# Kernel tuning notes

Measured on AMD Instinct MI355X. Metric: run time of the kernel, lower is better.

## Reference

```python
import jax, jax.numpy as jnp
import numpy as np

# dims (match init_kwargs / input_specs)
IN = 128      # input_size / num_features
GH = 512      # global_hidden_size
GL = 3        # global_nlayers
NH = 128      # effective noise hidden (DFRNN kwarg noise_nlayers, due to arg swap)
NL = 2        # effective noise layers (DFRNN kwarg noise_hidden_size, due to arg swap)
NF = 10       # n_global_factors
NT = 1024     # num_ts
T = 192       # num_periods


def _cell(x, W, bi, bh):
    # single LSTM step from zero state: c0=h0=0 => f-gate and W_hh drop out
    g = x @ W.T + bi + bh                      # [n, 4H]
    i, f, c, o = jnp.split(g, 4, axis=-1)      # torch gate order i,f,g,o
    cc = jax.nn.sigmoid(i) * jnp.tanh(c)
    return jax.nn.sigmoid(o) * jnp.tanh(cc)


def _stack(x, Wih0, bih0, bhh0, Wih, bih, bhh):
    h = _cell(x, Wih0, bih0, bhh0)
    for l in range(Wih.shape[0]):              # small fixed layer count
        h = _cell(h, Wih[l], bih[l], bhh[l])
    return h


def setup_inputs() -> dict:
    key = jax.random.key(0)
    ks = jax.random.split(key, 16)
    s = 0.05
    return {
        "X": jax.random.normal(ks[0], (NT, T, IN), jnp.float32),
        # global-factor LSTM params
        "g_Wih0": s * jax.random.normal(ks[1], (4 * GH, IN), jnp.float32),
        "g_bih0": s * jax.random.normal(ks[2], (4 * GH,), jnp.float32),
        "g_bhh0": s * jax.random.normal(ks[3], (4 * GH,), jnp.float32),
        "g_Wih": s * jax.random.normal(ks[4], (GL - 1, 4 * GH, GH), jnp.float32),
        "g_bih": s * jax.random.normal(ks[5], (GL - 1, 4 * GH), jnp.float32),
        "g_bhh": s * jax.random.normal(ks[6], (GL - 1, 4 * GH), jnp.float32),
        # embed linear (global_hidden_size -> n_global_factors)
        "e_W": s * jax.random.normal(ks[7], (NF, GH), jnp.float32),
        "e_b": s * jax.random.normal(ks[8], (NF,), jnp.float32),
        # noise LSTM params
        "n_Wih0": s * jax.random.normal(ks[9], (4 * NH, IN), jnp.float32),
        "n_bih0": s * jax.random.normal(ks[10], (4 * NH,), jnp.float32),
        "n_bhh0": s * jax.random.normal(ks[11], (4 * NH,), jnp.float32),
        "n_Wih": s * jax.random.normal(ks[12], (NL - 1, 4 * NH, NH), jnp.float32),
        "n_bih": s * jax.random.normal(ks[13], (NL - 1, 4 * NH), jnp.float32),
        "n_bhh": s * jax.random.normal(ks[14], (NL - 1, 4 * NH), jnp.float32),
        # noise affine head (NH -> 1)
        "a_W": s * jax.random.normal(ks[15], (1, NH), jnp.float32),
        "a_b": jnp.zeros((1,), jnp.float32),
    }


def reference(X, g_Wih0, g_bih0, g_bhh0, g_Wih, g_bih, g_bhh, e_W, e_b,
              n_Wih0, n_bih0, n_bhh0, n_Wih, n_bih, n_bhh, a_W, a_b):
    nt, t, f = X.shape
    Z = X.reshape(nt * t, f)                                   # all (ts, period) tokens, loop vectorized
    # DeepFactor branch: gt = relu(last-layer h), factor linear is dead code
    gt = jax.nn.relu(_stack(Z, g_Wih0, g_bih0, g_bhh0, g_Wih, g_bih, g_bhh))
    mu = (gt @ e_W.T + e_b).sum(axis=-1).reshape(nt, t)        # embed then sum over factors
    # Noise branch
    hn = jax.nn.relu(_stack(Z, n_Wih0, n_bih0, n_bhh0, n_Wih, n_bih, n_bhh))
    st = hn @ a_W.T + a_b                                      # [nt*t, 1]
    sigma = jnp.log1p(jnp.exp(st)).reshape(nt, t) + 1e-6       # log(1+exp) + eps
    return mu, sigma
```

## Files before the change

kernel.cpp:

```cpp
#include <hip/hip_runtime.h>

#define IN_F  128
#define GHID  512
#define NHID  128
#define NTOK  196608L
#define LDSP  520

#define L2E 1.4426950408889634f

typedef __attribute__((ext_vector_type(8))) short short8;
typedef __attribute__((ext_vector_type(4))) float floatx4;
typedef __attribute__((ext_vector_type(4))) float f4;

#define O_GW0 0L
#define O_GW1 196608L
#define O_GW2 983040L
#define O_NW0 1769472L
#define O_NW1 1818624L
#define NWS   1867776L
#define F_GB0 0
#define F_GB1 1536
#define F_GB2 3072
#define F_NB0 4608
#define F_NB1 4992
#define F_WE  5376
#define F_AW  5888
#define F_BE  6016
#define F_AB  6017

__device__ __forceinline__ unsigned short f2bf(float f) {
  unsigned int u = __float_as_uint(f);
  u += 0x7fffu + ((u >> 16) & 1u);
  return (unsigned short)(u >> 16);
}

__device__ __forceinline__ long srcoff(long pp, int H, int K) {
  long f = pp >> 9;
  int r = (int)(pp & 511);
  int ln = r >> 3, j = r & 7;
  int nKT = K >> 5, nCT = H >> 4;
  int tk = (int)(f % nKT);
  long t2 = f / nKT;
  int tn = (int)(t2 % nCT);
  int gate = (int)(t2 / nCT);
  int n = tn * 16 + (ln & 15);
  int k = tk * 32 + ((ln >> 4) << 3) + j;
  int go = (gate == 0) ? 0 : ((gate == 1) ? 2 * H : 3 * H);
  return (long)(go + n) * K + k;
}

__global__ void prep_kernel(
    const float* __restrict__ gW0, const float* __restrict__ gbi0, const float* __restrict__ gbh0,
    const float* __restrict__ gW,  const float* __restrict__ gbi,  const float* __restrict__ gbh,
    const float* __restrict__ eW,  const float* __restrict__ eb,
    const float* __restrict__ nW0, const float* __restrict__ nbi0, const float* __restrict__ nbh0,
    const float* __restrict__ nW,  const float* __restrict__ nbi,  const float* __restrict__ nbh,
    const float* __restrict__ aW,  const float* __restrict__ ab,
    unsigned short* __restrict__ wpk, float* __restrict__ fpk)
{
  long idx = (long)blockIdx.x * blockDim.x + threadIdx.x;
  if (idx < NWS) {
    const float* src;
    long off;
    if (idx < O_GW1)      { off = srcoff(idx - O_GW0, 512, 128); src = gW0; }
    else if (idx < O_GW2) { off = srcoff(idx - O_GW1, 512, 512); src = gW; }
    else if (idx < O_NW0) { off = srcoff(idx - O_GW2, 512, 512); src = gW + 1048576; }
    else if (idx < O_NW1) { off = srcoff(idx - O_NW0, 128, 128); src = nW0; }
    else                  { off = srcoff(idx - O_NW1, 128, 128); src = nW; }
    wpk[idx] = f2bf(src[off]);
    return;
  }
  long p = idx - NWS;
  if (p < 1536) { int g = (int)(p >> 9), n = (int)(p & 511);
    int o = (g == 0 ? 0 : (g == 1 ? 1024 : 1536)) + n;
    fpk[F_GB0 + p] = gbi0[o] + gbh0[o]; return; }
  p -= 1536;
  if (p < 1536) { int g = (int)(p >> 9), n = (int)(p & 511);
    int o = (g == 0 ? 0 : (g == 1 ? 1024 : 1536)) + n;
    fpk[F_GB1 + p] = gbi[o] + gbh[o]; return; }
  p -= 1536;
  if (p < 1536) { int g = (int)(p >> 9), n = (int)(p & 511);
    int o = (g == 0 ? 0 : (g == 1 ? 1024 : 1536)) + n;
    fpk[F_GB2 + p] = gbi[2048 + o] + gbh[2048 + o]; return; }
  p -= 1536;
  if (p < 384) { int g = (int)(p / 128), n = (int)(p % 128);
    int o = (g == 0 ? 0 : (g == 1 ? 256 : 384)) + n;
    fpk[F_NB0 + p] = nbi0[o] + nbh0[o]; return; }
  p -= 384;
  if (p < 384) { int g = (int)(p / 128), n = (int)(p % 128);
    int o = (g == 0 ? 0 : (g == 1 ? 256 : 384)) + n;
    fpk[F_NB1 + p] = nbi[o] + nbh[o]; return; }
  p -= 384;
  if (p < 512) { float s = 0.f;
    for (int f = 0; f < 10; ++f) s += eW[f * 512 + p];
    fpk[F_WE + p] = s; return; }
  p -= 512;
  if (p < 128) { fpk[F_AW + p] = aW[p]; return; }
  p -= 128;
  if (p == 0) { float s = 0.f; for (int f = 0; f < 10; ++f) s += eb[f]; fpk[F_BE] = s; return; }
  if (p == 1) { fpk[F_AB] = ab[0]; return; }
}

__device__ __forceinline__ float cell_h(float gi, float gc, float go) {
  float ei = __builtin_amdgcn_exp2f(gi * -L2E);
  float u  = __builtin_amdgcn_exp2f(gc * (2.0f * L2E));
  float eo = __builtin_amdgcn_exp2f(go * -L2E);
  float r1 = __builtin_amdgcn_rcpf((u + 1.f) * (1.f + ei));
  float cc = (u - 1.f) * r1;
  float s  = cc * cc;
  float num = cc * fmaf(10.f, s, 105.f);
  float den = fmaf(s, s + 45.f, 105.f);
  return num * __builtin_amdgcn_rcpf(den * (1.f + eo));
}

template <int K, int H, int TT, int CPW, int NW, int MODE>
__device__ __forceinline__ void layer_run(
    const unsigned short* __restrict__ sIn,
    unsigned short* __restrict__ sOut,
    const unsigned short* __restrict__ wp,
    const float* __restrict__ bias,
    const float* __restrict__ dotw,
    float* accVec,
    int colTile0, int tokBase, int lane)
{
  constexpr int nKT = K / 32;
  constexpr int nCT = H / 16;
#pragma unroll
  for (int cp = 0; cp < CPW; ++cp) {
    int tn = colTile0 + cp * NW;
    int colBase = tn * 16 + ((lane >> 4) << 2);
    const unsigned short* p0 = wp + (size_t)tn * nKT * 512 + lane * 8;
    const unsigned short* p1 = p0 + (size_t)nCT * nKT * 512;
    const unsigned short* p2 = p1 + (size_t)nCT * nKT * 512;
    short8 b0 = *(const short8*)(p0);
    short8 b1 = *(const short8*)(p1);
    short8 b2 = *(const short8*)(p2);
    f4 bi4 = *(const f4*)(bias + colBase);
    f4 bc4 = *(const f4*)(bias + H + colBase);
    f4 bo4 = *(const f4*)(bias + 2 * H + colBase);
    floatx4 acc[3][TT];
#pragma unroll
    for (int tt = 0; tt < TT; ++tt) {
      acc[0][tt] = (floatx4){bi4.x, bi4.y, bi4.z, bi4.w};
      acc[1][tt] = (floatx4){bc4.x, bc4.y, bc4.z, bc4.w};
      acc[2][tt] = (floatx4){bo4.x, bo4.y, bo4.z, bo4.w};
    }
    const unsigned short* aRow = sIn + (size_t)(tokBase + (lane & 15)) * LDSP + ((lane >> 4) << 3);
#pragma unroll 1
    for (int ks = 0; ks < nKT; ++ks) {
      int nks = (ks + 1 < nKT) ? (ks + 1) : ks;
      short8 nb0 = *(const short8*)(p0 + (size_t)nks * 512);
      short8 nb1 = *(const short8*)(p1 + (size_t)nks * 512);
      short8 nb2 = *(const short8*)(p2 + (size_t)nks * 512);
      short8 a[TT];
#pragma unroll
      for (int tt = 0; tt < TT; ++tt)
        a[tt] = *(const short8*)(aRow + (size_t)tt * 16 * LDSP + ks * 32);
#pragma unroll
      for (int tt = 0; tt < TT; ++tt) {
        acc[0][tt] = __builtin_amdgcn_mfma_f32_16x16x32_bf16(b0, a[tt], acc[0][tt], 0, 0, 0);
        acc[1][tt] = __builtin_amdgcn_mfma_f32_16x16x32_bf16(b1, a[tt], acc[1][tt], 0, 0, 0);
        acc[2][tt] = __builtin_amdgcn_mfma_f32_16x16x32_bf16(b2, a[tt], acc[2][tt], 0, 0, 0);
      }
      b0 = nb0; b1 = nb1; b2 = nb2;
    }
    f4 dw4;
    if constexpr (MODE == 1) dw4 = *(const f4*)(dotw + colBase);
#pragma unroll
    for (int tt = 0; tt < TT; ++tt) {
      int token = tokBase + tt * 16 + (lane & 15);
      if constexpr (MODE == 0) {
        ushort4 hw;
        hw.x = f2bf(cell_h(acc[0][tt][0], acc[1][tt][0], acc[2][tt][0]));
        hw.y = f2bf(cell_h(acc[0][tt][1], acc[1][tt][1], acc[2][tt][1]));
        hw.z = f2bf(cell_h(acc[0][tt][2], acc[1][tt][2], acc[2][tt][2]));
        hw.w = f2bf(cell_h(acc[0][tt][3], acc[1][tt][3], acc[2][tt][3]));
        *(ushort4*)&sOut[(size_t)token * LDSP + colBase] = hw;
      } else {
        float v = 0.f;
#pragma unroll
        for (int r = 0; r < 4; ++r) {
          float h = cell_h(acc[0][tt][r], acc[1][tt][r], acc[2][tt][r]);
          v = fmaf(fmaxf(h, 0.f), dw4[r], v);
        }
        v += __shfl_xor(v, 16);
        v += __shfl_xor(v, 32);
        if (lane < 16) atomicAdd(&accVec[token], v);
      }
    }
  }
}

__attribute__((amdgpu_waves_per_eu(4, 4)))
__global__ __launch_bounds__(1024) void dfrnn_main(
    const float* __restrict__ X,
    const unsigned short* __restrict__ wpk,
    const float* __restrict__ fpk,
    float* __restrict__ out)
{
  __shared__ __align__(16) unsigned short bufA[64 * LDSP];
  __shared__ __align__(16) unsigned short bufB[64 * LDSP];
  __shared__ float accMu[64];
  __shared__ float accSt[64];
  int tid = threadIdx.x;
  int wave = tid >> 6, lane = tid & 63;
  size_t blkTok = (size_t)blockIdx.x * 64;

  if (tid < 64) { accMu[tid] = 0.f; accSt[tid] = 0.f; }
  for (int i = tid; i < 64 * 32; i += 1024) {
    int row = i >> 5, c4 = i & 31;
    f4 v = __builtin_nontemporal_load((const f4*)(X + (blkTok + row) * 128 + c4 * 4));
    ushort4 b;
    b.x = f2bf(v.x); b.y = f2bf(v.y); b.z = f2bf(v.z); b.w = f2bf(v.w);
    *(ushort4*)&bufA[(size_t)row * LDSP + c4 * 4] = b;
  }
  __syncthreads();

  layer_run<128, 128, 2, 1, 8, 0>(bufA, bufA + 128, wpk + O_NW0, fpk + F_NB0,
                                  nullptr, nullptr, wave & 7, (wave >> 3) * 32, lane);
  __syncthreads();

  layer_run<128, 128, 2, 1, 8, 1>(bufA + 128, nullptr, wpk + O_NW1, fpk + F_NB1,
                                  fpk + F_AW, accSt, wave & 7, (wave >> 3) * 32, lane);
  layer_run<128, 512, 4, 2, 16, 0>(bufA, bufB, wpk + O_GW0, fpk + F_GB0,
                                   nullptr, nullptr, wave, 0, lane);
  __syncthreads();

  layer_run<512, 512, 4, 2, 16, 0>(bufB, bufA, wpk + O_GW1, fpk + F_GB1,
                                   nullptr, nullptr, wave, 0, lane);
  __syncthreads();

  layer_run<512, 512, 4, 2, 16, 1>(bufA, nullptr, wpk + O_GW2, fpk + F_GB2,
                                   fpk + F_WE, accMu, wave, 0, lane);
  __syncthreads();

  if (tid < 64) {
    float mu = accMu[tid] + fpk[F_BE];
    float st = accSt[tid] + fpk[F_AB];
    out[blkTok + tid] = mu;
    out[NTOK + blkTok + tid] = log1pf(__expf(st)) + 1e-6f;
  }
}

extern "C" void kernel_launch(void* const* d_in, const int* in_sizes, int n_in,
                              void* d_out, int out_size, void* d_ws, size_t ws_size,
                              hipStream_t stream) {
  const float* X     = (const float*)d_in[0];
  const float* gW0   = (const float*)d_in[1];
  const float* gbi0  = (const float*)d_in[2];
  const float* gbh0  = (const float*)d_in[3];
  const float* gW    = (const float*)d_in[4];
  const float* gbi   = (const float*)d_in[5];
  const float* gbh   = (const float*)d_in[6];
  const float* eW    = (const float*)d_in[7];
  const float* eb    = (const float*)d_in[8];
  const float* nW0   = (const float*)d_in[9];
  const float* nbi0  = (const float*)d_in[10];
  const float* nbh0  = (const float*)d_in[11];
  const float* nW    = (const float*)d_in[12];
  const float* nbi   = (const float*)d_in[13];
  const float* nbh   = (const float*)d_in[14];
  const float* aW    = (const float*)d_in[15];
  const float* ab    = (const float*)d_in[16];

  unsigned short* wpk = (unsigned short*)d_ws;
  float* fpk = (float*)((char*)d_ws + NWS * 2);

  long prepTotal = NWS + 1536 * 3 + 384 * 2 + 512 + 128 + 2;
  int prepBlocks = (int)((prepTotal + 255) / 256);
  prep_kernel<<<prepBlocks, 256, 0, stream>>>(gW0, gbi0, gbh0, gW, gbi, gbh, eW, eb,
                                              nW0, nbi0, nbh0, nW, nbi, nbh, aW, ab,
                                              wpk, fpk);
  dfrnn_main<<<3072, 1024, 0, stream>>>(X, wpk, fpk, (float*)d_out);
}
```

Before: 913.3 us.

## Register-block two column tiles per wave and halve block size

Each wave now computes two 16-column weight tiles against all token subtiles, so every LDS activation fragment feeds twice as many MFMAs. The block shrinks to 8 waves with a waves-per-EU hint of 2, and the activation fragment loads are prefetched one k-step ahead alongside the weights. The aim is to cut LDS read traffic and instruction overhead per MFMA, at the cost of higher register pressure and fewer resident waves for latency hiding.

New measurement: 960.2 us. 5.1% more time.

```diff
diff --git a/kernel.cpp b/kernel.cpp
--- a/kernel.cpp
+++ b/kernel.cpp
@@ -113,7 +113,7 @@
   return num * __builtin_amdgcn_rcpf(den * (1.f + eo));
 }
 
-template <int K, int H, int TT, int CPW, int NW, int MODE>
+template <int K, int H, int NT, int TT, int CPW, int CS, int TS, int MODE>
 __device__ __forceinline__ void layer_run(
     const unsigned short* __restrict__ sIn,
     unsigned short* __restrict__ sOut,
@@ -125,74 +125,99 @@
 {
   constexpr int nKT = K / 32;
   constexpr int nCT = H / 16;
+  constexpr size_t GS = (size_t)nCT * nKT * 512;
+  const unsigned short* wl = wp + lane * 8;
+  const unsigned short* aRow = sIn + (size_t)(tokBase + (lane & 15)) * LDSP + ((lane >> 4) << 3);
+
 #pragma unroll
   for (int cp = 0; cp < CPW; ++cp) {
-    int tn = colTile0 + cp * NW;
-    int colBase = tn * 16 + ((lane >> 4) << 2);
-    const unsigned short* p0 = wp + (size_t)tn * nKT * 512 + lane * 8;
-    const unsigned short* p1 = p0 + (size_t)nCT * nKT * 512;
-    const unsigned short* p2 = p1 + (size_t)nCT * nKT * 512;
-    short8 b0 = *(const short8*)(p0);
-    short8 b1 = *(const short8*)(p1);
-    short8 b2 = *(const short8*)(p2);
-    f4 bi4 = *(const f4*)(bias + colBase);
-    f4 bc4 = *(const f4*)(bias + H + colBase);
-    f4 bo4 = *(const f4*)(bias + 2 * H + colBase);
-    floatx4 acc[3][TT];
-#pragma unroll
-    for (int tt = 0; tt < TT; ++tt) {
-      acc[0][tt] = (floatx4){bi4.x, bi4.y, bi4.z, bi4.w};
-      acc[1][tt] = (floatx4){bc4.x, bc4.y, bc4.z, bc4.w};
-      acc[2][tt] = (floatx4){bo4.x, bo4.y, bo4.z, bo4.w};
+    const unsigned short* wb[NT];
+    floatx4 acc[NT][3][TT];
+#pragma unroll
+    for (int t = 0; t < NT; ++t) {
+      int tn = colTile0 + cp * CS + t * TS;
+      wb[t] = wl + (size_t)tn * nKT * 512;
+      int colBase = tn * 16 + ((lane >> 4) << 2);
+      f4 bi4 = *(const f4*)(bias + colBase);
+      f4 bc4 = *(const f4*)(bias + H + colBase);
+      f4 bo4 = *(const f4*)(bias + 2 * H + colBase);
+#pragma unroll
+      for (int tt = 0; tt < TT; ++tt) {
+        acc[t][0][tt] = (floatx4){bi4.x, bi4.y, bi4.z, bi4.w};
+        acc[t][1][tt] = (floatx4){bc4.x, bc4.y, bc4.z, bc4.w};
+        acc[t][2][tt] = (floatx4){bo4.x, bo4.y, bo4.z, bo4.w};
+      }
     }
-    const unsigned short* aRow = sIn + (size_t)(tokBase + (lane & 15)) * LDSP + ((lane >> 4) << 3);
+    short8 wc[NT][3], ac[TT];
+#pragma unroll
+    for (int t = 0; t < NT; ++t)
+#pragma unroll
+      for (int g = 0; g < 3; ++g)
+        wc[t][g] = *(const short8*)(wb[t] + g * GS);
+#pragma unroll
+    for (int tt = 0; tt < TT; ++tt)
+      ac[tt] = *(const short8*)(aRow + (size_t)tt * 16 * LDSP);
 #pragma unroll 1
     for (int ks = 0; ks < nKT; ++ks) {
-      int nks = (ks + 1 < nKT) ? (ks + 1) : ks;
-      short8 nb0 = *(const short8*)(p0 + (size_t)nks * 512);
-      short8 nb1 = *(const short8*)(p1 + (size_t)nks * 512);
-      short8 nb2 = *(const short8*)(p2 + (size_t)nks * 512);
-      short8 a[TT];
+      int nks = (ks + 1 < nKT) ? ks + 1 : ks;
+      short8 wn[NT][3], an[TT];
+#pragma unroll
+      for (int t = 0; t < NT; ++t)
+#pragma unroll
+        for (int g = 0; g < 3; ++g)
+          wn[t][g] = *(const short8*)(wb[t] + g * GS + (size_t)nks * 512);
 #pragma unroll
       for (int tt = 0; tt < TT; ++tt)
-        a[tt] = *(const short8*)(aRow + (size_t)tt * 16 * LDSP + ks * 32);
+        an[tt] = *(const short8*)(aRow + (size_t)tt * 16 * LDSP + nks * 32);
+#pragma unroll
+      for (int tt = 0; tt < TT; ++tt)
+#pragma unroll
+        for (int t = 0; t < NT; ++t) {
+          acc[t][0][tt] = __builtin_amdgcn_mfma_f32_16x16x32_bf16(wc[t][0], ac[tt], acc[t][0][tt], 0, 0, 0);
+          acc[t][1][tt] = __builtin_amdgcn_mfma_f32_16x16x32_bf16(wc[t][1], ac[tt], acc[t][1][tt], 0, 0, 0);
+          acc[t][2][tt] = __builtin_amdgcn_mfma_f32_16x16x32_bf16(wc[t][2], ac[tt], acc[t][2][tt], 0, 0, 0);
+        }
+#pragma unroll
+      for (int t = 0; t < NT; ++t)
+#pragma unroll
+        for (int g = 0; g < 3; ++g) wc[t][g] = wn[t][g];
+#pragma unroll
+      for (int tt = 0; tt < TT; ++tt) ac[tt] = an[tt];
+    }
+#pragma unroll
+    for (int t = 0; t < NT; ++t) {
+      int tn = colTile0 + cp * CS + t * TS;
+      int colBase = tn * 16 + ((lane >> 4) << 2);
+      f4 dw4;
+      if constexpr (MODE == 1) dw4 = *(const f4*)(dotw + colBase);
 #pragma unroll
       for (int tt = 0; tt < TT; ++tt) {
-        acc[0][tt] = __builtin_amdgcn_mfma_f32_16x16x32_bf16(b0, a[tt], acc[0][tt], 0, 0, 0);
-        acc[1][tt] = __builtin_amdgcn_mfma_f32_16x16x32_bf16(b1, a[tt], acc[1][tt], 0, 0, 0);
-        acc[2][tt] = __builtin_amdgcn_mfma_f32_16x16x32_bf16(b2, a[tt], acc[2][tt], 0, 0, 0);
-      }
-      b0 = nb0; b1 = nb1; b2 = nb2;
-    }
-    f4 dw4;
-    if constexpr (MODE == 1) dw4 = *(const f4*)(dotw + colBase);
-#pragma unroll
-    for (int tt = 0; tt < TT; ++tt) {
-      int token = tokBase + tt * 16 + (lane & 15);
-      if constexpr (MODE == 0) {
-        ushort4 hw;
-        hw.x = f2bf(cell_h(acc[0][tt][0], acc[1][tt][0], acc[2][tt][0]));
-        hw.y = f2bf(cell_h(acc[0][tt][1], acc[1][tt][1], acc[2][tt][1]));
-        hw.z = f2bf(cell_h(acc[0][tt][2], acc[1][tt][2], acc[2][tt][2]));
-        hw.w = f2bf(cell_h(acc[0][tt][3], acc[1][tt][3], acc[2][tt][3]));
-        *(ushort4*)&sOut[(size_t)token * LDSP + colBase] = hw;
-      } else {
-        float v = 0.f;
-#pragma unroll
-        for (int r = 0; r < 4; ++r) {
-          float h = cell_h(acc[0][tt][r], acc[1][tt][r], acc[2][tt][r]);
-          v = fmaf(fmaxf(h, 0.f), dw4[r], v);
+        int token = tokBase + tt * 16 + (lane & 15);
+        if constexpr (MODE == 0) {
+          ushort4 hw;
+          hw.x = f2bf(cell_h(acc[t][0][tt][0], acc[t][1][tt][0], acc[t][2][tt][0]));
+          hw.y = f2bf(cell_h(acc[t][0][tt][1], acc[t][1][tt][1], acc[t][2][tt][1]));
+          hw.z = f2bf(cell_h(acc[t][0][tt][2], acc[t][1][tt][2], acc[t][2][tt][2]));
+          hw.w = f2bf(cell_h(acc[t][0][tt][3], acc[t][1][tt][3], acc[t][2][tt][3]));
+          *(ushort4*)&sOut[(size_t)token * LDSP + colBase] = hw;
+        } else {
+          float v = 0.f;
+#pragma unroll
+          for (int r = 0; r < 4; ++r) {
+            float h = cell_h(acc[t][0][tt][r], acc[t][1][tt][r], acc[t][2][tt][r]);
+            v = fmaf(fmaxf(h, 0.f), dw4[r], v);
+          }
+          v += __shfl_xor(v, 16);
+          v += __shfl_xor(v, 32);
+          if (lane < 16) atomicAdd(&accVec[token], v);
         }
-        v += __shfl_xor(v, 16);
-        v += __shfl_xor(v, 32);
-        if (lane < 16) atomicAdd(&accVec[token], v);
       }
     }
   }
 }
 
-__attribute__((amdgpu_waves_per_eu(4, 4)))
-__global__ __launch_bounds__(1024) void dfrnn_main(
+__attribute__((amdgpu_waves_per_eu(2, 2)))
+__global__ __launch_bounds__(512) void dfrnn_main(
     const float* __restrict__ X,
     const unsigned short* __restrict__ wpk,
     const float* __restrict__ fpk,
@@ -207,7 +232,7 @@
   size_t blkTok = (size_t)blockIdx.x * 64;
 
   if (tid < 64) { accMu[tid] = 0.f; accSt[tid] = 0.f; }
-  for (int i = tid; i < 64 * 32; i += 1024) {
+  for (int i = tid; i < 64 * 32; i += 512) {
     int row = i >> 5, c4 = i & 31;
     f4 v = __builtin_nontemporal_load((const f4*)(X + (blkTok + row) * 128 + c4 * 4));
     ushort4 b;
@@ -216,22 +241,22 @@
   }
   __syncthreads();
 
-  layer_run<128, 128, 2, 1, 8, 0>(bufA, bufA + 128, wpk + O_NW0, fpk + F_NB0,
-                                  nullptr, nullptr, wave & 7, (wave >> 3) * 32, lane);
-  __syncthreads();
-
-  layer_run<128, 128, 2, 1, 8, 1>(bufA + 128, nullptr, wpk + O_NW1, fpk + F_NB1,
-                                  fpk + F_AW, accSt, wave & 7, (wave >> 3) * 32, lane);
-  layer_run<128, 512, 4, 2, 16, 0>(bufA, bufB, wpk + O_GW0, fpk + F_GB0,
-                                   nullptr, nullptr, wave, 0, lane);
-  __syncthreads();
-
-  layer_run<512, 512, 4, 2, 16, 0>(bufB, bufA, wpk + O_GW1, fpk + F_GB1,
-                                   nullptr, nullptr, wave, 0, lane);
-  __syncthreads();
-
-  layer_run<512, 512, 4, 2, 16, 1>(bufA, nullptr, wpk + O_GW2, fpk + F_GB2,
-                                   fpk + F_WE, accMu, wave, 0, lane);
+  layer_run<128, 128, 1, 4, 1, 0, 0, 0>(bufA, bufA + 128, wpk + O_NW0, fpk + F_NB0,
+                                        nullptr, nullptr, wave, 0, lane);
+  __syncthreads();
+
+  layer_run<128, 128, 1, 4, 1, 0, 0, 1>(bufA + 128, nullptr, wpk + O_NW1, fpk + F_NB1,
+                                        fpk + F_AW, accSt, wave, 0, lane);
+  layer_run<128, 512, 2, 4, 2, 16, 8, 0>(bufA, bufB, wpk + O_GW0, fpk + F_GB0,
+                                         nullptr, nullptr, wave, 0, lane);
+  __syncthreads();
+
+  layer_run<512, 512, 2, 4, 2, 16, 8, 0>(bufB, bufA, wpk + O_GW1, fpk + F_GB1,
+                                         nullptr, nullptr, wave, 0, lane);
+  __syncthreads();
+
+  layer_run<512, 512, 2, 4, 2, 16, 8, 1>(bufA, nullptr, wpk + O_GW2, fpk + F_GB2,
+                                         fpk + F_WE, accMu, wave, 0, lane);
   __syncthreads();
 
   if (tid < 64) {
@@ -271,5 +296,5 @@
   prep_kernel<<<prepBlocks, 256, 0, stream>>>(gW0, gbi0, gbh0, gW, gbi, gbh, eW, eb,
                                               nW0, nbi0, nbh0, nW, nbi, nbh, aW, ab,
                                               wpk, fpk);
-  dfrnn_main<<<3072, 1024, 0, stream>>>(X, wpk, fpk, (float*)d_out);
-}
+  dfrnn_main<<<3072, 512, 0, stream>>>(X, wpk, fpk, (float*)d_out);
+}
```
